# Kernel optimization log

Measured on AMD Instinct MI355X. Metric: run time of the kernel, lower is better.

## Reference

```python
import jax, jax.numpy as jnp
import numpy as np

B, T, F, H = 128, 1024, 256, 512  # batch, seq_len (input_dims[0]), features (input_dims[1]), rnn_size


def _lstm(xWb, U, reverse=False, return_sequences=False):
    """Keras-semantics LSTM. xWb: [B,T,4H] = x @ W + b precomputed. Gate order i,f,g,o."""
    Hn = U.shape[0]
    xs = jnp.swapaxes(xWb, 0, 1)  # [T,B,4H] for scan over time
    h0 = jnp.zeros((xWb.shape[0], Hn), xWb.dtype)
    c0 = h0

    def step(carry, xw):
        h, c = carry
        z = xw + h @ U  # [B,4H]
        i, f, g, o = jnp.split(z, 4, axis=-1)
        i = jax.nn.sigmoid(i)
        f = jax.nn.sigmoid(f)
        g = jnp.tanh(g)
        o = jax.nn.sigmoid(o)
        c = f * c + i * g
        h = o * jnp.tanh(c)
        return (h, c), h

    (hT, _), hs = jax.lax.scan(step, (h0, c0), xs, reverse=reverse)
    if return_sequences:
        return jnp.swapaxes(hs, 0, 1)  # [B,T,H]
    return hT  # [B,H] final state (for reverse=True this is the state after t=0)


def setup_inputs() -> dict:
    key = jax.random.key(0)
    ks = jax.random.split(key, 9)
    g = lambda k, shape: (jax.random.normal(k, shape, jnp.float32) * 0.05)
    return {
        "x": jax.random.uniform(ks[0], (B, T, F), jnp.float32),
        # encoder forward-direction LSTM
        "Wf": g(ks[1], (F, 4 * H)), "Uf": g(ks[2], (H, 4 * H)), "bf": jnp.zeros((4 * H,), jnp.float32),
        # encoder backward-direction LSTM
        "Wb": g(ks[3], (F, 4 * H)), "Ub": g(ks[4], (H, 4 * H)), "bb": jnp.zeros((4 * H,), jnp.float32),
        # decoder LSTM (input is concat latent, 2H wide)
        "Wd": g(ks[5], (2 * H, 4 * H)), "Ud": g(ks[6], (H, 4 * H)), "bd": jnp.zeros((4 * H,), jnp.float32),
        # TimeDistributed Dense
        "Wo": g(ks[7], (H, F)), "bo": jnp.zeros((F,), jnp.float32),
    }


def reference(x, Wf, Uf, bf, Wb, Ub, bb, Wd, Ud, bd, Wo, bo):
    # Encoder: Bidirectional(LSTM(H)) -> concat final states [B, 2H]
    h_fwd = _lstm(x @ Wf + bf, Uf, reverse=False)
    h_bwd = _lstm(x @ Wb + bb, Ub, reverse=True)
    latent = jnp.concatenate([h_fwd, h_bwd], axis=-1)  # [B, 2H]
    # Decoder: RepeatVector(T) -> LSTM(H, return_sequences) -> TimeDistributed(Dense(F))
    rep = jnp.broadcast_to(latent[:, None, :], (x.shape[0], x.shape[1], 2 * H))  # [B,T,2H]
    dec = _lstm(rep @ Wd + bd, Ud, return_sequences=True)  # [B,T,H]
    return dec @ Wo + bo  # [B,T,F]
```

## Files before the change

kernel.cpp:

```cpp
#include <hip/hip_runtime.h>
#include <stdint.h>

typedef unsigned short u16;
typedef short bf16x8 __attribute__((ext_vector_type(8)));
typedef float f32x4  __attribute__((ext_vector_type(4)));
typedef unsigned short u16x8 __attribute__((ext_vector_type(8)));
typedef unsigned int   u32x4 __attribute__((ext_vector_type(4)));

__device__ __forceinline__ u16 f2bf(float f) {
  uint32_t u = __float_as_uint(f);
  return (u16)((u + 0x7FFFu + ((u >> 16) & 1u)) >> 16);
}
__device__ __forceinline__ float fsig(float x) {
  x = fminf(fmaxf(x, -30.f), 30.f);
  return __builtin_amdgcn_rcpf(1.f + __builtin_amdgcn_exp2f(-1.44269504088896f * x));
}
__device__ __forceinline__ float ftanhf(float x) {
  x = fminf(fmaxf(x, -10.f), 10.f);
  float e = __builtin_amdgcn_exp2f(2.88539008177793f * x);
  return (e - 1.f) * __builtin_amdgcn_rcpf(e + 1.f);
}

__device__ __forceinline__ int flag_load(const int* p) {
  int v;
  asm volatile("global_load_dword %0, %1, off sc0 sc1\n\ts_waitcnt vmcnt(0)"
               : "=v"(v) : "v"(p) : "memory");
  return v;
}
__device__ __forceinline__ void flag_store(int* p, int v) {
  asm volatile("global_store_dword %0, %1, off sc0 sc1" :: "v"(p), "v"(v) : "memory");
}
__device__ __forceinline__ uint4 ld_coh_x4(const u16* p) {
  uint4 v;
  asm volatile("global_load_dwordx4 %0, %1, off sc0 sc1" : "=v"(v) : "v"(p) : "memory");
  return v;
}
__device__ __forceinline__ void st_coh_x4(u16* p, u32x4 v) {
  asm volatile("global_store_dwordx4 %0, %1, off sc0 sc1" :: "v"(p), "v"(v) : "memory");
}
__device__ __forceinline__ uint4 ld_x4(const float* p) {
  uint4 v;
  asm volatile("global_load_dwordx4 %0, %1, off" : "=v"(v) : "v"(p) : "memory");
  return v;
}
__device__ __forceinline__ void wait_vm0() {
  asm volatile("s_waitcnt vmcnt(0)" ::: "memory");
}
__device__ __forceinline__ void wait_vm4() {
  asm volatile("s_waitcnt vmcnt(4)" ::: "memory");
}
__device__ __forceinline__ bf16x8 pin_frag(const u16* p) {
  uint4 v;
  asm volatile("global_load_dwordx4 %0, %1, off" : "=v"(v) : "v"(p));
  return __builtin_bit_cast(bf16x8, v);
}
__device__ __forceinline__ void poll_flag(const int* fp, int target) {
  int spins = 0;
  while (flag_load(fp) < target) {
    __builtin_amdgcn_s_sleep(1);
    if (++spins > 200000) break;
  }
}

__global__ void prep_kernel(const float* __restrict__ Wf, const float* __restrict__ Uf, const float* __restrict__ bf,
                            const float* __restrict__ Wb, const float* __restrict__ Ub, const float* __restrict__ bb,
                            const float* __restrict__ Wd, const float* __restrict__ Ud, const float* __restrict__ bd,
                            const float* __restrict__ Wo,
                            u16* __restrict__ encF, u16* __restrict__ encB,
                            u16* __restrict__ udF, u16* __restrict__ wdF, u16* __restrict__ woF,
                            float* __restrict__ biasF, float* __restrict__ biasB, float* __restrict__ biasD,
                            int* __restrict__ flagsAll)
{
  constexpr int NC_ENC = 128 * 24 * 64;
  constexpr int NC_UD  = 128 * 16 * 64;
  constexpr int NC_WD  = 128 * 32 * 64;
  constexpr int NC_WO  = 16 * 16 * 64;
  constexpr int B1 = 2 * NC_ENC;
  constexpr int B2 = B1 + NC_UD;
  constexpr int B3 = B2 + NC_WD;
  constexpr int B4 = B3 + NC_WO;
  constexpr int B5 = B4 + 768;
  constexpr int TOTAL = B5 + 64;

  for (int idx = blockIdx.x * 256 + threadIdx.x; idx < TOTAL; idx += gridDim.x * 256) {
    if (idx < B1) {
      int d = idx / NC_ENC;
      int r = idx - d * NC_ENC;
      int ntg = r / 1536;
      int rem = r - ntg * 1536;
      int kt = rem >> 6, lane = rem & 63;
      int np = ntg * 16 + (lane & 15);
      int col = (np & 3) * 512 + (np >> 2);
      int kb = kt * 32 + (lane >> 4) * 8;
      const float* W = d ? Wb : Wf;
      const float* U = d ? Ub : Uf;
      u16* dst = (d ? encB : encF) + (size_t)r * 8;
      if (kb < 256) {
        const float* s = W + (size_t)kb * 2048 + col;
#pragma unroll
        for (int e = 0; e < 8; ++e) dst[e] = f2bf(s[(size_t)e * 2048]);
      } else {
        const float* s = U + (size_t)(kb - 256) * 2048 + col;
#pragma unroll
        for (int e = 0; e < 8; ++e) dst[e] = f2bf(s[(size_t)e * 2048]);
      }
    } else if (idx < B2) {
      int r = idx - B1;
      int ntg = r / 1024;
      int rem = r - ntg * 1024;
      int kt = rem >> 6, lane = rem & 63;
      int np = ntg * 16 + (lane & 15);
      int col = (np & 3) * 512 + (np >> 2);
      int kb = kt * 32 + (lane >> 4) * 8;
      const float* s = Ud + (size_t)kb * 2048 + col;
      u16* dst = udF + (size_t)r * 8;
#pragma unroll
      for (int e = 0; e < 8; ++e) dst[e] = f2bf(s[(size_t)e * 2048]);
    } else if (idx < B3) {
      int r = idx - B2;
      int ntg = r / 2048;
      int rem = r - ntg * 2048;
      int kt = rem >> 6, lane = rem & 63;
      int np = ntg * 16 + (lane & 15);
      int col = (np & 3) * 512 + (np >> 2);
      int kb = kt * 32 + (lane >> 4) * 8;
      const float* s = Wd + (size_t)kb * 2048 + col;
      u16* dst = wdF + (size_t)r * 8;
#pragma unroll
      for (int e = 0; e < 8; ++e) dst[e] = f2bf(s[(size_t)e * 2048]);
    } else if (idx < B4) {
      int r = idx - B3;
      int nt = r / 1024;
      int rem = r - nt * 1024;
      int kt = rem >> 6, lane = rem & 63;
      int col = nt * 16 + (lane & 15);
      int kb = kt * 32 + (lane >> 4) * 8;
      const float* s = Wo + (size_t)kb * 256 + col;
      u16* dst = woF + (size_t)r * 8;
#pragma unroll
      for (int e = 0; e < 8; ++e) dst[e] = f2bf(s[(size_t)e * 256]);
    } else if (idx < B5) {
      int r = idx - B4;
      int which = r >> 8;
      int j0 = (r & 255) * 8;
      const float* src = (which == 0) ? bf : (which == 1) ? bb : bd;
      float* dstb = (which == 0) ? biasF : (which == 1) ? biasB : biasD;
#pragma unroll
      for (int e = 0; e < 8; ++e) {
        int np = j0 + e;
        dstb[np] = src[(np & 3) * 512 + (np >> 2)];
      }
    } else {
      int r = idx - B5;
#pragma unroll
      for (int e = 0; e < 8; ++e) flagsAll[r * 8 + e] = 0;
    }
  }
}


__global__ __launch_bounds__(256, 1) void enc_kernel(
    const float* __restrict__ x,
    const u16* __restrict__ encF, const u16* __restrict__ encB,
    const float* __restrict__ biasF, const float* __restrict__ biasB,
    float* __restrict__ latent, u16* __restrict__ hbuf, int* __restrict__ flags)
{
  const int bid = blockIdx.x;
  const int g   = bid & 15;
  const int wgi = bid >> 4;
  const int dir = g >> 3;
  const int rowBase = (g & 7) * 16;
  const int tid = threadIdx.x;
  const int lane = tid & 63;
  const int wave = tid >> 6;
  const int l15 = lane & 15;
  const int lk  = lane >> 4;

  __shared__ __attribute__((aligned(16))) u16   xlds[2][16][264];
  __shared__ __attribute__((aligned(16))) u16   Alds[16][520];
  __shared__ __attribute__((aligned(16))) float zlds[4][2][16][20];
  __shared__ __attribute__((aligned(16))) u16   hlds[4][16][8];

  const u16* wsrc = dir ? encB : encF;
  bf16x8 Breg[2][24];
#pragma unroll
  for (int n = 0; n < 2; ++n) {
    const int ntg = wgi * 8 + wave * 2 + n;
    const u16* fb = wsrc + (size_t)(ntg * 1536 + lane) * 8;
#pragma unroll
    for (int kt = 0; kt < 24; ++kt)
      Breg[n][kt] = pin_frag(fb + kt * 512);
  }
  wait_vm0();
  __builtin_amdgcn_sched_barrier(0);

  const float* bias = dir ? biasB : biasF;
  float bias_r[2];
  bias_r[0] = bias[(wgi * 8 + wave * 2 + 0) * 16 + l15];
  bias_r[1] = bias[(wgi * 8 + wave * 2 + 1) * 16 + l15];

  u16* myH = hbuf + (size_t)g * 16384;
  int* myFlags = flags + g * 16;
  const int* myPollFlag = &myFlags[tid >> 4];
  const int xr = tid >> 4, xc = tid & 15;
  const int cb = tid >> 2;
  const int cr0 = (tid & 3) * 4;

  {
    const int t0 = dir ? 1023 : 0;
    const float* xp = x + ((size_t)(rowBase + xr) * 1024 + t0) * 256 + xc * 16;
    float4 f0 = *(const float4*)xp;
    float4 f1 = *(const float4*)(xp + 4);
    float4 f2 = *(const float4*)(xp + 8);
    float4 f3 = *(const float4*)(xp + 12);
    u16x8 a, b;
    a[0]=f2bf(f0.x); a[1]=f2bf(f0.y); a[2]=f2bf(f0.z); a[3]=f2bf(f0.w);
    a[4]=f2bf(f1.x); a[5]=f2bf(f1.y); a[6]=f2bf(f1.z); a[7]=f2bf(f1.w);
    b[0]=f2bf(f2.x); b[1]=f2bf(f2.y); b[2]=f2bf(f2.z); b[3]=f2bf(f2.w);
    b[4]=f2bf(f3.x); b[5]=f2bf(f3.y); b[6]=f2bf(f3.z); b[7]=f2bf(f3.w);
    *(u16x8*)&xlds[0][xr][xc * 16] = a;
    *(u16x8*)&xlds[0][xr][xc * 16 + 8] = b;
  }
  __syncthreads();

  float cc0 = 0.f, cc1 = 0.f;

  for (int s = 0; s < 1024; ++s) {
    f32x4 acc0 = {bias_r[0], bias_r[0], bias_r[0], bias_r[0]};
    f32x4 acc1 = {bias_r[1], bias_r[1], bias_r[1], bias_r[1]};
#pragma unroll
    for (int kt = 0; kt < 8; ++kt) {
      bf16x8 av = *(const bf16x8*)&xlds[s & 1][l15][kt * 32 + lk * 8];
      acc0 = __builtin_amdgcn_mfma_f32_16x16x32_bf16(av, Breg[0][kt], acc0, 0, 0, 0);
      acc1 = __builtin_amdgcn_mfma_f32_16x16x32_bf16(av, Breg[1][kt], acc1, 0, 0, 0);
    }

    const int sn = (s + 1 < 1024) ? s + 1 : 1023;
    const int tn = dir ? (1023 - sn) : sn;
    const float* xp = x + ((size_t)(rowBase + xr) * 1024 + tn) * 256 + xc * 16;
    uint4 xq0, xq1, xq2, xq3;

    if (s > 0) {
      poll_flag(myPollFlag, s);
      const u16* hs = myH + ((s - 1) & 1) * 8192 + cb * 128 + cr0 * 8;
      uint4 h0 = ld_coh_x4(hs);
      uint4 h1 = ld_coh_x4(hs + 8);
      uint4 h2 = ld_coh_x4(hs + 16);
      uint4 h3 = ld_coh_x4(hs + 24);
      xq0 = ld_x4(xp);
      xq1 = ld_x4(xp + 4);
      xq2 = ld_x4(xp + 8);
      xq3 = ld_x4(xp + 12);
      wait_vm4();
      __builtin_amdgcn_sched_barrier(0);
      *(uint4*)&Alds[cr0][cb * 8]     = h0;
      *(uint4*)&Alds[cr0 + 1][cb * 8] = h1;
      *(uint4*)&Alds[cr0 + 2][cb * 8] = h2;
      *(uint4*)&Alds[cr0 + 3][cb * 8] = h3;
      __syncthreads();
#pragma unroll
      for (int kt = 0; kt < 16; ++kt) {
        bf16x8 av = *(const bf16x8*)&Alds[l15][kt * 32 + lk * 8];
        acc0 = __builtin_amdgcn_mfma_f32_16x16x32_bf16(av, Breg[0][kt + 8], acc0, 0, 0, 0);
        acc1 = __builtin_amdgcn_mfma_f32_16x16x32_bf16(av, Breg[1][kt + 8], acc1, 0, 0, 0);
      }
    } else {
      xq0 = ld_x4(xp);
      xq1 = ld_x4(xp + 4);
      xq2 = ld_x4(xp + 8);
      xq3 = ld_x4(xp + 12);
    }

#pragma unroll
    for (int r = 0; r < 4; ++r) {
      zlds[wave][0][lk * 4 + r][l15] = acc0[r];
      zlds[wave][1][lk * 4 + r][l15] = acc1[r];
    }
    asm volatile("s_waitcnt lgkmcnt(0)" ::: "memory");
    float4 g0 = *(const float4*)&zlds[wave][0][l15][lk * 4];
    float4 g1 = *(const float4*)&zlds[wave][1][l15][lk * 4];
    float hv0, hv1;
    { float iv = fsig(g0.x), fv = fsig(g0.y), gg = ftanhf(g0.z), ov = fsig(g0.w);
      cc0 = fv * cc0 + iv * gg;  hv0 = ov * ftanhf(cc0); }
    { float iv = fsig(g1.x), fv = fsig(g1.y), gg = ftanhf(g1.z), ov = fsig(g1.w);
      cc1 = fv * cc1 + iv * gg;  hv1 = ov * ftanhf(cc1); }

    wait_vm0();
    __builtin_amdgcn_sched_barrier(0);
    {
      float4 f0 = __builtin_bit_cast(float4, xq0);
      float4 f1 = __builtin_bit_cast(float4, xq1);
      float4 f2 = __builtin_bit_cast(float4, xq2);
      float4 f3 = __builtin_bit_cast(float4, xq3);
      u16x8 a, b;
      a[0]=f2bf(f0.x); a[1]=f2bf(f0.y); a[2]=f2bf(f0.z); a[3]=f2bf(f0.w);
      a[4]=f2bf(f1.x); a[5]=f2bf(f1.y); a[6]=f2bf(f1.z); a[7]=f2bf(f1.w);
      b[0]=f2bf(f2.x); b[1]=f2bf(f2.y); b[2]=f2bf(f2.z); b[3]=f2bf(f2.w);
      b[4]=f2bf(f3.x); b[5]=f2bf(f3.y); b[6]=f2bf(f3.z); b[7]=f2bf(f3.w);
      *(u16x8*)&xlds[(s + 1) & 1][xr][xc * 16] = a;
      *(u16x8*)&xlds[(s + 1) & 1][xr][xc * 16 + 8] = b;
    }

    if (s < 1023) {
      hlds[wave][l15][lk]     = f2bf(hv0);
      hlds[wave][l15][lk + 4] = f2bf(hv1);
      asm volatile("s_waitcnt lgkmcnt(0)" ::: "memory");
      if (lane < 16) {
        const u32x4 c = *(const u32x4*)&hlds[wave][lane][0];
        u16* hw = myH + (s & 1) * 8192 + (wgi * 4 + wave) * 128 + lane * 8;
        st_coh_x4(hw, c);
      }
    } else {
      float* lp = latent + (size_t)(rowBase + l15) * 1024 + dir * 512 + wgi * 32 + wave * 8 + lk;
      lp[0] = hv0;
      lp[4] = hv1;
    }

    wait_vm0();
    __syncthreads();
    if (tid == 0 && s < 1023) flag_store(&myFlags[wgi], s + 1);
  }
}

__global__ __launch_bounds__(256, 1) void dec_kernel(
    const float* __restrict__ latent,
    const u16* __restrict__ udF, const u16* __restrict__ wdF, const u16* __restrict__ woF,
    const float* __restrict__ biasD, const float* __restrict__ bo,
    float* __restrict__ out, u16* __restrict__ hbuf, int* __restrict__ flags)
{
  const int bid = blockIdx.x;
  const int g   = bid & 7;
  const int wgi = bid >> 3;
  const int rowBase = g * 16;
  const int tid = threadIdx.x;
  const int lane = tid & 63;
  const int wave = tid >> 6;
  const int l15 = lane & 15;
  const int lk  = lane >> 4;

  __shared__ __attribute__((aligned(16))) u16   Llds[16][1032];
  __shared__ __attribute__((aligned(16))) u16   Alds[16][520];
  __shared__ __attribute__((aligned(16))) float zlds[4][2][16][20];
  __shared__ __attribute__((aligned(16))) u16   hlds[4][16][8];

#pragma unroll
  for (int c8 = 0; c8 < 8; ++c8) {
    const int idx = tid + c8 * 256;
    const int rr = idx >> 7, cf = idx & 127;
    const float* lp = latent + (size_t)(rowBase + rr) * 1024 + cf * 8;
    float4 v0 = *(const float4*)lp;
    float4 v1 = *(const float4*)(lp + 4);
    u16x8 tv;
    tv[0]=f2bf(v0.x); tv[1]=f2bf(v0.y); tv[2]=f2bf(v0.z); tv[3]=f2bf(v0.w);
    tv[4]=f2bf(v1.x); tv[5]=f2bf(v1.y); tv[6]=f2bf(v1.z); tv[7]=f2bf(v1.w);
    *(u16x8*)&Llds[rr][cf * 8] = tv;
  }
  __syncthreads();

  f32x4 xwd[2];
#pragma unroll
  for (int n = 0; n < 2; ++n) {
    const int ntg = wgi * 8 + wave * 2 + n;
    const float br = biasD[ntg * 16 + l15];
    f32x4 xw = {br, br, br, br};
    const u16* wf = wdF + (size_t)(ntg * 2048 + lane) * 8;
#pragma unroll
    for (int kt = 0; kt < 32; ++kt) {
      bf16x8 b = *(const bf16x8*)(wf + kt * 512);
      bf16x8 a = *(const bf16x8*)&Llds[l15][kt * 32 + lk * 8];
      xw = __builtin_amdgcn_mfma_f32_16x16x32_bf16(a, b, xw, 0, 0, 0);
    }
    xwd[n] = xw;
  }

  bf16x8 Bu[2][16];
#pragma unroll
  for (int n = 0; n < 2; ++n) {
    const int ntg = wgi * 8 + wave * 2 + n;
    const u16* ub = udF + (size_t)(ntg * 1024 + lane) * 8;
#pragma unroll
    for (int kt = 0; kt < 16; ++kt)
      Bu[n][kt] = pin_frag(ub + kt * 512);
  }
  bf16x8 Bo[16];
  if (wave == 0) {
    const u16* ob = woF + (size_t)(wgi * 1024 + lane) * 8;
#pragma unroll
    for (int kt = 0; kt < 16; ++kt)
      Bo[kt] = pin_frag(ob + kt * 512);
  }
  wait_vm0();
  __builtin_amdgcn_sched_barrier(0);
  const float bo_r = bo[wgi * 16 + l15];

  u16* myH = hbuf + (size_t)g * 16384;
  int* myFlags = flags + g * 16;
  const int* myPollFlag = &myFlags[tid >> 4];
  const int cb = tid >> 2;
  const int cr0 = (tid & 3) * 4;

  float cc0 = 0.f, cc1 = 0.f;

  for (int t = 0; t < 1024; ++t) {
    f32x4 acc0 = xwd[0], acc1 = xwd[1];

    if (t > 0) {
      poll_flag(myPollFlag, t);
      const u16* hs = myH + ((t - 1) & 1) * 8192 + cb * 128 + cr0 * 8;
      uint4 h0 = ld_coh_x4(hs);
      uint4 h1 = ld_coh_x4(hs + 8);
      uint4 h2 = ld_coh_x4(hs + 16);
      uint4 h3 = ld_coh_x4(hs + 24);
      wait_vm0();
      __builtin_amdgcn_sched_barrier(0);
      *(uint4*)&Alds[cr0][cb * 8]     = h0;
      *(uint4*)&Alds[cr0 + 1][cb * 8] = h1;
      *(uint4*)&Alds[cr0 + 2][cb * 8] = h2;
      *(uint4*)&Alds[cr0 + 3][cb * 8] = h3;
      __syncthreads();
#pragma unroll
      for (int kt = 0; kt < 16; ++kt) {
        bf16x8 av = *(const bf16x8*)&Alds[l15][kt * 32 + lk * 8];
        acc0 = __builtin_amdgcn_mfma_f32_16x16x32_bf16(av, Bu[0][kt], acc0, 0, 0, 0);
        acc1 = __builtin_amdgcn_mfma_f32_16x16x32_bf16(av, Bu[1][kt], acc1, 0, 0, 0);
      }
    }

#pragma unroll
    for (int r = 0; r < 4; ++r) {
      zlds[wave][0][lk * 4 + r][l15] = acc0[r];
      zlds[wave][1][lk * 4 + r][l15] = acc1[r];
    }
    asm volatile("s_waitcnt lgkmcnt(0)" ::: "memory");
    float4 g0 = *(const float4*)&zlds[wave][0][l15][lk * 4];
    float4 g1 = *(const float4*)&zlds[wave][1][l15][lk * 4];
    float hv0, hv1;
    { float iv = fsig(g0.x), fv = fsig(g0.y), gg = ftanhf(g0.z), ov = fsig(g0.w);
      cc0 = fv * cc0 + iv * gg;  hv0 = ov * ftanhf(cc0); }
    { float iv = fsig(g1.x), fv = fsig(g1.y), gg = ftanhf(g1.z), ov = fsig(g1.w);
      cc1 = fv * cc1 + iv * gg;  hv1 = ov * ftanhf(cc1); }

    {
      hlds[wave][l15][lk]     = f2bf(hv0);
      hlds[wave][l15][lk + 4] = f2bf(hv1);
      asm volatile("s_waitcnt lgkmcnt(0)" ::: "memory");
      if (lane < 16) {
        const u32x4 c = *(const u32x4*)&hlds[wave][lane][0];
        u16* hw = myH + (t & 1) * 8192 + (wgi * 4 + wave) * 128 + lane * 8;
        st_coh_x4(hw, c);
      }
      wait_vm0();
      __syncthreads();
      if (tid == 0) flag_store(&myFlags[wgi], t + 1);
    }

    if (t > 0 && wave == 0) {
      f32x4 od = {bo_r, bo_r, bo_r, bo_r};
#pragma unroll
      for (int kt = 0; kt < 16; ++kt) {
        bf16x8 a = *(const bf16x8*)&Alds[l15][kt * 32 + lk * 8];
        od = __builtin_amdgcn_mfma_f32_16x16x32_bf16(a, Bo[kt], od, 0, 0, 0);
      }
#pragma unroll
      for (int r = 0; r < 4; ++r)
        out[((size_t)(rowBase + lk * 4 + r) * 1024 + (t - 1)) * 256 + wgi * 16 + l15] = od[r];
    }
    __syncthreads();
  }

  poll_flag(myPollFlag, 1024);
  {
    const u16* hs = myH + 8192 + cb * 128 + cr0 * 8;
    uint4 h0 = ld_coh_x4(hs);
    uint4 h1 = ld_coh_x4(hs + 8);
    uint4 h2 = ld_coh_x4(hs + 16);
    uint4 h3 = ld_coh_x4(hs + 24);
    wait_vm0();
    __builtin_amdgcn_sched_barrier(0);
    *(uint4*)&Alds[cr0][cb * 8]     = h0;
    *(uint4*)&Alds[cr0 + 1][cb * 8] = h1;
    *(uint4*)&Alds[cr0 + 2][cb * 8] = h2;
    *(uint4*)&Alds[cr0 + 3][cb * 8] = h3;
    __syncthreads();
    if (wave == 0) {
      f32x4 od = {bo_r, bo_r, bo_r, bo_r};
#pragma unroll
      for (int kt = 0; kt < 16; ++kt) {
        bf16x8 a = *(const bf16x8*)&Alds[l15][kt * 32 + lk * 8];
        od = __builtin_amdgcn_mfma_f32_16x16x32_bf16(a, Bo[kt], od, 0, 0, 0);
      }
#pragma unroll
      for (int r = 0; r < 4; ++r)
        out[((size_t)(rowBase + lk * 4 + r) * 1024 + 1023) * 256 + wgi * 16 + l15] = od[r];
    }
  }
}

extern "C" void kernel_launch(void* const* d_in, const int* in_sizes, int n_in,
                              void* d_out, int out_size, void* d_ws, size_t ws_size,
                              hipStream_t stream)
{
  const float* x  = (const float*)d_in[0];
  const float* Wf = (const float*)d_in[1];
  const float* Uf = (const float*)d_in[2];
  const float* bf = (const float*)d_in[3];
  const float* Wb = (const float*)d_in[4];
  const float* Ub = (const float*)d_in[5];
  const float* bb = (const float*)d_in[6];
  const float* Wd = (const float*)d_in[7];
  const float* Ud = (const float*)d_in[8];
  const float* bd = (const float*)d_in[9];
  const float* Wo = (const float*)d_in[10];
  const float* bo = (const float*)d_in[11];

  if (ws_size < 14182400) return;

  char* ws = (char*)d_ws;
  u16*  encF   = (u16*)(ws + 0);
  u16*  encB   = (u16*)(ws + 3145728);
  u16*  udF    = (u16*)(ws + 6291456);
  u16*  wdF    = (u16*)(ws + 8388608);
  u16*  woF    = (u16*)(ws + 12582912);
  float* biasF = (float*)(ws + 12845056);
  float* biasB = (float*)(ws + 12853248);
  float* biasD = (float*)(ws + 12861440);
  float* latent= (float*)(ws + 12869632);
  u16*  hbufE  = (u16*)(ws + 13393920);
  u16*  hbufD  = (u16*)(ws + 13918208);
  int*  flagsE = (int*)(ws + 14180352);
  int*  flagsD = (int*)(ws + 14181376);

  prep_kernel<<<256, 256, 0, stream>>>(Wf, Uf, bf, Wb, Ub, bb, Wd, Ud, bd, Wo,
                                       encF, encB, udF, wdF, woF,
                                       biasF, biasB, biasD, flagsE);
  enc_kernel<<<256, 256, 0, stream>>>(x, encF, encB, biasF, biasB, latent, hbufE, flagsE);
  dec_kernel<<<128, 256, 0, stream>>>(latent, udF, wdF, woF, biasD, bo,
                                      (float*)d_out, hbufD, flagsD);
}
```

Measured before the change: 5.778 ms.

## Use per-wave completion flags and double-buffered LDS to drop per-step barriers

Each wave now publishes its own progress flag right after writing its hidden-state slice, replacing the single per-workgroup flag that needed a __syncthreads first. Consumers poll the finer-grained flags. The encoder issues its h store and flag earlier so they overlap the next x conversion. The decoder double-buffers its A tile in LDS so the trailing barrier each step can go. The spin-wait also drops s_sleep for tighter polling, at the cost of more memory traffic, and the flag arrays are moved and resized in the workspace.

After: 6.552 ms. +13.4%, slower.

```diff
diff --git a/kernel.cpp b/kernel.cpp
--- a/kernel.cpp
+++ b/kernel.cpp
@@ -57,8 +57,7 @@
 __device__ __forceinline__ void poll_flag(const int* fp, int target) {
   int spins = 0;
   while (flag_load(fp) < target) {
-    __builtin_amdgcn_s_sleep(1);
-    if (++spins > 200000) break;
+    if (++spins > 300000) break;
   }
 }
 
@@ -69,7 +68,7 @@
                             u16* __restrict__ encF, u16* __restrict__ encB,
                             u16* __restrict__ udF, u16* __restrict__ wdF, u16* __restrict__ woF,
                             float* __restrict__ biasF, float* __restrict__ biasB, float* __restrict__ biasD,
-                            int* __restrict__ flagsAll)
+                            int* __restrict__ flagsE, int* __restrict__ flagsD)
 {
   constexpr int NC_ENC = 128 * 24 * 64;
   constexpr int NC_UD  = 128 * 16 * 64;
@@ -80,7 +79,8 @@
   constexpr int B3 = B2 + NC_WD;
   constexpr int B4 = B3 + NC_WO;
   constexpr int B5 = B4 + 768;
-  constexpr int TOTAL = B5 + 64;
+  constexpr int B6 = B5 + 128;
+  constexpr int TOTAL = B6 + 64;
 
   for (int idx = blockIdx.x * 256 + threadIdx.x; idx < TOTAL; idx += gridDim.x * 256) {
     if (idx < B1) {
@@ -150,10 +150,14 @@
         int np = j0 + e;
         dstb[np] = src[(np & 3) * 512 + (np >> 2)];
       }
+    } else if (idx < B6) {
+      int r = idx - B5;
+#pragma unroll
+      for (int e = 0; e < 8; ++e) flagsE[r * 8 + e] = 0;
     } else {
-      int r = idx - B5;
-#pragma unroll
-      for (int e = 0; e < 8; ++e) flagsAll[r * 8 + e] = 0;
+      int r = idx - B6;
+#pragma unroll
+      for (int e = 0; e < 8; ++e) flagsD[r * 8 + e] = 0;
     }
   }
 }
@@ -200,8 +204,9 @@
   bias_r[1] = bias[(wgi * 8 + wave * 2 + 1) * 16 + l15];
 
   u16* myH = hbuf + (size_t)g * 16384;
-  int* myFlags = flags + g * 16;
-  const int* myPollFlag = &myFlags[tid >> 4];
+  int* myFlags = flags + g * 64;
+  const int* myPollFlag = &myFlags[tid >> 2];
+  const int myFlagIdx = wgi * 4 + wave;
   const int xr = tid >> 4, xc = tid & 15;
   const int cb = tid >> 2;
   const int cr0 = (tid & 3) * 4;
@@ -285,8 +290,24 @@
     { float iv = fsig(g1.x), fv = fsig(g1.y), gg = ftanhf(g1.z), ov = fsig(g1.w);
       cc1 = fv * cc1 + iv * gg;  hv1 = ov * ftanhf(cc1); }
 
+    if (s < 1023) {
+      hlds[wave][l15][lk]     = f2bf(hv0);
+      hlds[wave][l15][lk + 4] = f2bf(hv1);
+      asm volatile("s_waitcnt lgkmcnt(0)" ::: "memory");
+      if (lane < 16) {
+        const u32x4 c = *(const u32x4*)&hlds[wave][lane][0];
+        u16* hw = myH + (s & 1) * 8192 + (wgi * 4 + wave) * 128 + lane * 8;
+        st_coh_x4(hw, c);
+      }
+    } else {
+      float* lp = latent + (size_t)(rowBase + l15) * 1024 + dir * 512 + wgi * 32 + wave * 8 + lk;
+      lp[0] = hv0;
+      lp[4] = hv1;
+    }
     wait_vm0();
     __builtin_amdgcn_sched_barrier(0);
+    if (lane == 0 && s < 1023) flag_store(&myFlags[myFlagIdx], s + 1);
+
     {
       float4 f0 = __builtin_bit_cast(float4, xq0);
       float4 f1 = __builtin_bit_cast(float4, xq1);
@@ -300,25 +321,7 @@
       *(u16x8*)&xlds[(s + 1) & 1][xr][xc * 16] = a;
       *(u16x8*)&xlds[(s + 1) & 1][xr][xc * 16 + 8] = b;
     }
-
-    if (s < 1023) {
-      hlds[wave][l15][lk]     = f2bf(hv0);
-      hlds[wave][l15][lk + 4] = f2bf(hv1);
-      asm volatile("s_waitcnt lgkmcnt(0)" ::: "memory");
-      if (lane < 16) {
-        const u32x4 c = *(const u32x4*)&hlds[wave][lane][0];
-        u16* hw = myH + (s & 1) * 8192 + (wgi * 4 + wave) * 128 + lane * 8;
-        st_coh_x4(hw, c);
-      }
-    } else {
-      float* lp = latent + (size_t)(rowBase + l15) * 1024 + dir * 512 + wgi * 32 + wave * 8 + lk;
-      lp[0] = hv0;
-      lp[4] = hv1;
-    }
-
-    wait_vm0();
     __syncthreads();
-    if (tid == 0 && s < 1023) flag_store(&myFlags[wgi], s + 1);
   }
 }
 
@@ -339,7 +342,7 @@
   const int lk  = lane >> 4;
 
   __shared__ __attribute__((aligned(16))) u16   Llds[16][1032];
-  __shared__ __attribute__((aligned(16))) u16   Alds[16][520];
+  __shared__ __attribute__((aligned(16))) u16   Alds[2][16][520];
   __shared__ __attribute__((aligned(16))) float zlds[4][2][16][20];
   __shared__ __attribute__((aligned(16))) u16   hlds[4][16][8];
 
@@ -394,8 +397,9 @@
   const float bo_r = bo[wgi * 16 + l15];
 
   u16* myH = hbuf + (size_t)g * 16384;
-  int* myFlags = flags + g * 16;
-  const int* myPollFlag = &myFlags[tid >> 4];
+  int* myFlags = flags + g * 64;
+  const int* myPollFlag = &myFlags[tid >> 2];
+  const int myFlagIdx = wgi * 4 + wave;
   const int cb = tid >> 2;
   const int cr0 = (tid & 3) * 4;
 
@@ -413,14 +417,14 @@
       uint4 h3 = ld_coh_x4(hs + 24);
       wait_vm0();
       __builtin_amdgcn_sched_barrier(0);
-      *(uint4*)&Alds[cr0][cb * 8]     = h0;
-      *(uint4*)&Alds[cr0 + 1][cb * 8] = h1;
-      *(uint4*)&Alds[cr0 + 2][cb * 8] = h2;
-      *(uint4*)&Alds[cr0 + 3][cb * 8] = h3;
+      *(uint4*)&Alds[t & 1][cr0][cb * 8]     = h0;
+      *(uint4*)&Alds[t & 1][cr0 + 1][cb * 8] = h1;
+      *(uint4*)&Alds[t & 1][cr0 + 2][cb * 8] = h2;
+      *(uint4*)&Alds[t & 1][cr0 + 3][cb * 8] = h3;
       __syncthreads();
 #pragma unroll
       for (int kt = 0; kt < 16; ++kt) {
-        bf16x8 av = *(const bf16x8*)&Alds[l15][kt * 32 + lk * 8];
+        bf16x8 av = *(const bf16x8*)&Alds[t & 1][l15][kt * 32 + lk * 8];
         acc0 = __builtin_amdgcn_mfma_f32_16x16x32_bf16(av, Bu[0][kt], acc0, 0, 0, 0);
         acc1 = __builtin_amdgcn_mfma_f32_16x16x32_bf16(av, Bu[1][kt], acc1, 0, 0, 0);
       }
@@ -450,22 +454,21 @@
         st_coh_x4(hw, c);
       }
       wait_vm0();
-      __syncthreads();
-      if (tid == 0) flag_store(&myFlags[wgi], t + 1);
+      __builtin_amdgcn_sched_barrier(0);
+      if (lane == 0) flag_store(&myFlags[myFlagIdx], t + 1);
     }
 
     if (t > 0 && wave == 0) {
       f32x4 od = {bo_r, bo_r, bo_r, bo_r};
 #pragma unroll
       for (int kt = 0; kt < 16; ++kt) {
-        bf16x8 a = *(const bf16x8*)&Alds[l15][kt * 32 + lk * 8];
+        bf16x8 a = *(const bf16x8*)&Alds[t & 1][l15][kt * 32 + lk * 8];
         od = __builtin_amdgcn_mfma_f32_16x16x32_bf16(a, Bo[kt], od, 0, 0, 0);
       }
 #pragma unroll
       for (int r = 0; r < 4; ++r)
         out[((size_t)(rowBase + lk * 4 + r) * 1024 + (t - 1)) * 256 + wgi * 16 + l15] = od[r];
     }
-    __syncthreads();
   }
 
   poll_flag(myPollFlag, 1024);
@@ -477,16 +480,16 @@
     uint4 h3 = ld_coh_x4(hs + 24);
     wait_vm0();
     __builtin_amdgcn_sched_barrier(0);
-    *(uint4*)&Alds[cr0][cb * 8]     = h0;
-    *(uint4*)&Alds[cr0 + 1][cb * 8] = h1;
-    *(uint4*)&Alds[cr0 + 2][cb * 8] = h2;
-    *(uint4*)&Alds[cr0 + 3][cb * 8] = h3;
+    *(uint4*)&Alds[0][cr0][cb * 8]     = h0;
+    *(uint4*)&Alds[0][cr0 + 1][cb * 8] = h1;
+    *(uint4*)&Alds[0][cr0 + 2][cb * 8] = h2;
+    *(uint4*)&Alds[0][cr0 + 3][cb * 8] = h3;
     __syncthreads();
     if (wave == 0) {
       f32x4 od = {bo_r, bo_r, bo_r, bo_r};
 #pragma unroll
       for (int kt = 0; kt < 16; ++kt) {
-        bf16x8 a = *(const bf16x8*)&Alds[l15][kt * 32 + lk * 8];
+        bf16x8 a = *(const bf16x8*)&Alds[0][l15][kt * 32 + lk * 8];
         od = __builtin_amdgcn_mfma_f32_16x16x32_bf16(a, Bo[kt], od, 0, 0, 0);
       }
 #pragma unroll
@@ -527,12 +530,12 @@
   float* latent= (float*)(ws + 12869632);
   u16*  hbufE  = (u16*)(ws + 13393920);
   u16*  hbufD  = (u16*)(ws + 13918208);
-  int*  flagsE = (int*)(ws + 14180352);
-  int*  flagsD = (int*)(ws + 14181376);
+  int*  flagsE = (int*)(ws + 13918208);
+  int*  flagsD = (int*)(ws + 14180352);
 
   prep_kernel<<<256, 256, 0, stream>>>(Wf, Uf, bf, Wb, Ub, bb, Wd, Ud, bd, Wo,
                                        encF, encB, udF, wdF, woF,
-                                       biasF, biasB, biasD, flagsE);
+                                       biasF, biasB, biasD, flagsE, flagsD);
   enc_kernel<<<256, 256, 0, stream>>>(x, encF, encB, biasF, biasB, latent, hbufE, flagsE);
   dec_kernel<<<128, 256, 0, stream>>>(latent, udF, wdF, woF, biasD, bo,
                                       (float*)d_out, hbufD, flagsD);
```
